# Kernel tuning notes

Hardware: AMD Instinct MI355X
Metric: run time of the kernel (lower is better)

Reference implementation:

```python
import jax, jax.numpy as jnp
import numpy as np

# Module constants (match init_kwargs / DCNv4 defaults)
N, C, H, W = 4, 256, 128, 128
G = 4                       # DCNv4 default group
KS = 3                      # kernel_size
K = KS * KS                 # 9 sampling points per group
Cg = C // G                 # channels per group
PAD_OFF = int(np.ceil(G * K * 3 / 8) * 8)  # 112, padded offset_mask dim
EPS = 1e-5                  # BatchNorm2d eps


def setup_inputs() -> dict:
    key = jax.random.key(0)
    ks = jax.random.split(key, 6)
    s = 0.05
    return {
        "x": jax.random.normal(ks[0], (N, C, H, W), jnp.float32),
        "conv_w": jax.random.normal(ks[1], (C, C, 1, 1), jnp.float32) * s,
        "bn1_gamma": jnp.ones((C,), jnp.float32),
        "bn1_beta": jnp.zeros((C,), jnp.float32),
        "bn1_mean": jnp.zeros((C,), jnp.float32),
        "bn1_var": jnp.ones((C,), jnp.float32),
        "value_w": jax.random.normal(ks[2], (C, C), jnp.float32) * s,
        "value_b": jnp.zeros((C,), jnp.float32),
        "offset_w": jax.random.normal(ks[3], (PAD_OFF, C), jnp.float32) * s,
        "offset_b": jnp.zeros((PAD_OFF,), jnp.float32),
        "out_w": jax.random.normal(ks[4], (C, C), jnp.float32) * s,
        "out_b": jnp.zeros((C,), jnp.float32),
        "bn2_gamma": jnp.ones((C,), jnp.float32),
        "bn2_beta": jnp.zeros((C,), jnp.float32),
        "bn2_mean": jnp.zeros((C,), jnp.float32),
        "bn2_var": jnp.ones((C,), jnp.float32),
    }


def _bilinear(v, lh, lw):
    """Bilinear sample v:(N,H,W,G,Cg) at float locs lh/lw:(N,H,W,G); zero outside."""
    n, h, w, g, c = v.shape
    h0 = jnp.floor(lh)
    w0 = jnp.floor(lw)
    dh = lh - h0
    dw = lw - w0
    h0i = h0.astype(jnp.int32)
    w0i = w0.astype(jnp.int32)
    vf = v.reshape(n, h * w, g, c)

    def gather(hh, ww):
        valid = (hh >= 0) & (hh < h) & (ww >= 0) & (ww < w)
        idx = jnp.clip(hh, 0, h - 1) * w + jnp.clip(ww, 0, w - 1)
        out = jnp.take_along_axis(vf, idx.reshape(n, h * w, g)[..., None], axis=1)
        return out.reshape(n, h, w, g, c) * valid[..., None].astype(v.dtype)

    w00 = (1 - dh) * (1 - dw)
    w01 = (1 - dh) * dw
    w10 = dh * (1 - dw)
    w11 = dh * dw
    return (gather(h0i, w0i) * w00[..., None]
            + gather(h0i, w0i + 1) * w01[..., None]
            + gather(h0i + 1, w0i) * w10[..., None]
            + gather(h0i + 1, w0i + 1) * w11[..., None])


def _bn(x_nchw, gamma, beta, mean, var):
    scale = (gamma / jnp.sqrt(var + EPS))[None, :, None, None]
    return x_nchw * scale + (beta - mean * gamma / jnp.sqrt(var + EPS))[None, :, None, None]


def reference(x, conv_w, bn1_gamma, bn1_beta, bn1_mean, bn1_var,
              value_w, value_b, offset_w, offset_b, out_w, out_b,
              bn2_gamma, bn2_beta, bn2_mean, bn2_var):
    n, _, h, w = x.shape
    # ---- Conv(c1,c2,k=1): 1x1 conv (no bias) + BN + SiLU ----
    y = jnp.einsum('nchw,oc->nohw', x, conv_w[:, :, 0, 0])
    y = jax.nn.silu(_bn(y, bn1_gamma, bn1_beta, bn1_mean, bn1_var))

    # ---- DCNv4 on (N, L, C) tokens ----
    t = y.transpose(0, 2, 3, 1)                      # (N,H,W,C)
    v = t @ value_w.T + value_b                      # value_proj
    om = t @ offset_w.T + offset_b                   # (N,H,W,112)
    om = om[..., : G * K * 3].reshape(n, h, w, G, K * 3)
    off = om[..., : 2 * K].reshape(n, h, w, G, K, 2) # (dx, dy) per point
    mask = om[..., 2 * K:]                           # (N,H,W,G,K), no softmax in v4
    v = v.reshape(n, h, w, G, Cg)

    hi = jnp.arange(h, dtype=jnp.float32)[None, :, None, None]
    wi = jnp.arange(w, dtype=jnp.float32)[None, None, :, None]
    out = jnp.zeros_like(v)
    for k in range(K):  # fixed small kernel loop (9 points)
        i, j = divmod(k, KS)
        lh = hi + (i - 1) + off[..., k, 1]           # stride=1, pad=1, dil=1
        lw = wi + (j - 1) + off[..., k, 0]           # offset_scale=1.0
        out = out + mask[..., k, None] * _bilinear(v, lh, lw)

    o = out.reshape(n, h, w, C) @ out_w.T + out_b    # output_proj
    o = o.transpose(0, 3, 1, 2)                      # back to NCHW

    # ---- final BN + SiLU ----
    return jax.nn.silu(_bn(o, bn2_gamma, bn2_beta, bn2_mean, bn2_var))
```

## Files before the change

### kernel.cpp

```cpp
#include <hip/hip_runtime.h>
#include <cstdint>

typedef unsigned short u16;
typedef unsigned int   u32;
typedef __attribute__((ext_vector_type(8))) __bf16 bf16x8;
typedef __attribute__((ext_vector_type(2))) float  f32x2;
typedef __attribute__((ext_vector_type(4))) float  f32x4;
typedef __attribute__((ext_vector_type(4))) u32    u32x4;

#define N_IMG 4
#define C_DIM 256
#define H_DIM 128
#define W_DIM 128
#define HW    (H_DIM * W_DIM)
#define M_TOT (N_IMG * HW)
#define CG    64
#define PADOFF 112
#define EPSV  1e-5f

__device__ __forceinline__ u16 f2b(float f) {
  u32 u = __float_as_uint(f);
  u += 0x7fffu + ((u >> 16) & 1u);
  return (u16)(u >> 16);
}

__device__ __forceinline__ void async_cp16(const void* g, void* l) {
  __builtin_amdgcn_global_load_lds(
      (const __attribute__((address_space(1))) void*)g,
      (__attribute__((address_space(3))) void*)l, 16, 0, 0);
}

__global__ __launch_bounds__(256) void cast_all(
    const float* __restrict__ a0, u16* __restrict__ o0,
    const float* __restrict__ a1, u16* __restrict__ o1,
    const float* __restrict__ a2, u16* __restrict__ o2,
    const float* __restrict__ a3, u16* __restrict__ o3) {
  int i = blockIdx.x * 256 + threadIdx.x;
  const float* in; u16* out; int base;
  if (i < 16384)      { in = a0; out = o0; base = 0; }
  else if (i < 32768) { in = a1; out = o1; base = 16384; }
  else if (i < 39936) { in = a2; out = o2; base = 32768; }
  else                { in = a3; out = o3; base = 39936; }
  int j = i - base;
  f32x4 v = reinterpret_cast<const f32x4*>(in)[j];
  u32 lo = (u32)f2b(v[0]) | ((u32)f2b(v[1]) << 16);
  u32 hi = (u32)f2b(v[2]) | ((u32)f2b(v[3]) << 16);
  reinterpret_cast<u32*>(out)[2 * j]     = lo;
  reinterpret_cast<u32*>(out)[2 * j + 1] = hi;
}

__global__ __launch_bounds__(256) void gemm_conv(
    const float* __restrict__ X, const u16* __restrict__ B,
    u16* __restrict__ Cb,
    const float* __restrict__ gamma, const float* __restrict__ beta,
    const float* __restrict__ mean, const float* __restrict__ var) {
  constexpr int BM = 128, BK = 32;
  __shared__ __align__(16) u16 As[BM * BK];
  __shared__ __align__(16) u16 Bs[BM * BK];
  const int tid  = threadIdx.x;
  const int lane = tid & 63;
  const int wave = tid >> 6;
  const int quad = lane >> 4;
  const int l16  = lane & 15;
  const int bm = blockIdx.x * BM;
  const int bn = blockIdx.y * BM;
  const int wm = (wave & 1) * 64;
  const int wn = (wave >> 1) * 64;
  const int img = bm >> 14;
  const int hw0 = bm & (HW - 1);
  const int p2  = (tid & 63) * 2;
  const int hh  = tid >> 6;
  const float* xb = X + (size_t)img * C_DIM * HW + hw0 + p2;

  f32x4 acc[4][4] = {};

  for (int ko = 0; ko < C_DIM; ko += BK) {
    float a0[8], a1[8];
#pragma unroll
    for (int j = 0; j < 8; ++j) {
      f32x2 fv = *reinterpret_cast<const f32x2*>(
          xb + (size_t)(ko + hh * 8 + j) * HW);
      a0[j] = fv.x; a1[j] = fv.y;
    }
    u32x4 w0, w1;
#pragma unroll
    for (int j = 0; j < 4; ++j) {
      w0[j] = (u32)f2b(a0[2 * j]) | ((u32)f2b(a0[2 * j + 1]) << 16);
      w1[j] = (u32)f2b(a1[2 * j]) | ((u32)f2b(a1[2 * j + 1]) << 16);
    }
    {
      u32x4* Ar = reinterpret_cast<u32x4*>(As);
      int sw = hh ^ ((p2 >> 1) & 3);
      Ar[p2 * 4 + sw]       = w0;
      Ar[(p2 + 1) * 4 + sw] = w1;
    }
#pragma unroll
    for (int it = 0; it < 2; ++it) {
      int chunk = it * 256 + tid;
      int r  = chunk >> 2;
      int kk = (chunk & 3) << 3;
      async_cp16(B + (size_t)(bn + r) * C_DIM + (ko + kk),
                 Bs + (size_t)(it * 256 + wave * 64) * 8);
    }
    __syncthreads();
    const bf16x8* Apf = reinterpret_cast<const bf16x8*>(As);
    const bf16x8* Bpf = reinterpret_cast<const bf16x8*>(Bs);
    bf16x8 af[4], bfr[4];
#pragma unroll
    for (int mi = 0; mi < 4; ++mi) {
      int r = wm + mi * 16 + l16;
      af[mi] = Apf[r * 4 + (quad ^ ((r >> 1) & 3))];
    }
#pragma unroll
    for (int ni = 0; ni < 4; ++ni)
      bfr[ni] = Bpf[(wn + ni * 16 + l16) * 4 + quad];
#pragma unroll
    for (int mi = 0; mi < 4; ++mi)
#pragma unroll
      for (int ni = 0; ni < 4; ++ni)
        acc[mi][ni] = __builtin_amdgcn_mfma_f32_16x16x32_bf16(
            af[mi], bfr[ni], acc[mi][ni], 0, 0, 0);
    __syncthreads();
  }

#pragma unroll
  for (int ni = 0; ni < 4; ++ni) {
    int n = bn + wn + ni * 16 + l16;
    float sc = gamma[n] * rsqrtf(var[n] + EPSV);
    float sh = beta[n] - mean[n] * sc;
#pragma unroll
    for (int mi = 0; mi < 4; ++mi) {
      int mrow = bm + wm + mi * 16 + quad * 4;
#pragma unroll
      for (int i = 0; i < 4; ++i) {
        float y = acc[mi][ni][i] * sc + sh;
        y = y / (1.f + __expf(-y));
        Cb[(size_t)(mrow + i) * C_DIM + n] = f2b(y);
      }
    }
  }
}

template <int MODE>
__global__ __launch_bounds__(256) void gemm_ep(
    const u16* __restrict__ A, const u16* __restrict__ B,
    u16* __restrict__ Cb, float* __restrict__ Cf, int K, int Nreal,
    const float* __restrict__ bias, const float* __restrict__ bias2,
    const float* __restrict__ gamma, const float* __restrict__ beta,
    const float* __restrict__ mean, const float* __restrict__ var) {
  constexpr int BM = 128, BK = 64;
  __shared__ __align__(16) u16 As[BM * BK];
  __shared__ __align__(16) u16 Bs[BM * BK];
  const int tid  = threadIdx.x;
  const int lane = tid & 63;
  const int wave = tid >> 6;
  const int quad = lane >> 4;
  const int l16  = lane & 15;
  const int bm = blockIdx.x * BM;
  const int bn = blockIdx.y * BM;
  const int wm = (wave & 1) * 64;
  const int wn = (wave >> 1) * 64;

  f32x4 acc[4][4] = {};

  for (int ko = 0; ko < K; ko += BK) {
#pragma unroll
    for (int it = 0; it < 4; ++it) {
      int chunk = it * 256 + tid;
      int r  = chunk >> 3;
      int j  = chunk & 7;
      int kk = (j ^ (r & 7)) << 3;
      const u16* ga = A + (size_t)(bm + r) * K + (ko + kk);
      int br = bn + r; if (br >= Nreal) br = Nreal - 1;
      const u16* gb = B + (size_t)br * K + (ko + kk);
      u16* la = As + (size_t)(it * 256 + wave * 64) * 8;
      u16* lb = Bs + (size_t)(it * 256 + wave * 64) * 8;
      async_cp16(ga, la);
      async_cp16(gb, lb);
    }
    __syncthreads();
    const bf16x8* Ap = reinterpret_cast<const bf16x8*>(As);
    const bf16x8* Bp = reinterpret_cast<const bf16x8*>(Bs);
#pragma unroll
    for (int ks = 0; ks < 2; ++ks) {
      bf16x8 af[4], bfr[4];
#pragma unroll
      for (int mi = 0; mi < 4; ++mi) {
        int row = wm + mi * 16 + l16;
        af[mi] = Ap[row * 8 + ((ks * 4 + quad) ^ (row & 7))];
      }
#pragma unroll
      for (int ni = 0; ni < 4; ++ni) {
        int row = wn + ni * 16 + l16;
        bfr[ni] = Bp[row * 8 + ((ks * 4 + quad) ^ (row & 7))];
      }
#pragma unroll
      for (int mi = 0; mi < 4; ++mi)
#pragma unroll
        for (int ni = 0; ni < 4; ++ni)
          acc[mi][ni] = __builtin_amdgcn_mfma_f32_16x16x32_bf16(
              af[mi], bfr[ni], acc[mi][ni], 0, 0, 0);
    }
    __syncthreads();
  }

#pragma unroll
  for (int ni = 0; ni < 4; ++ni) {
    int n = bn + wn + ni * 16 + l16;
    if constexpr (MODE == 3) {
      float sc = gamma[n] * rsqrtf(var[n] + EPSV);
      float sh = beta[n] - mean[n] * sc + bias[n] * sc;
#pragma unroll
      for (int mi = 0; mi < 4; ++mi) {
        int mrow = bm + wm + mi * 16 + quad * 4;
        int img = mrow >> 14;
        int hw  = mrow & (HW - 1);
        f32x4 y;
#pragma unroll
        for (int i = 0; i < 4; ++i) {
          float z = acc[mi][ni][i] * sc + sh;
          y[i] = z / (1.f + __expf(-z));
        }
        *reinterpret_cast<f32x4*>(
            Cf + (size_t)img * C_DIM * HW + (size_t)n * HW + hw) = y;
      }
    } else {
      if (bn < C_DIM) {
        float sh = bias[n];
#pragma unroll
        for (int mi = 0; mi < 4; ++mi) {
          int mrow = bm + wm + mi * 16 + quad * 4;
#pragma unroll
          for (int i = 0; i < 4; ++i)
            Cb[(size_t)(mrow + i) * C_DIM + n] = f2b(acc[mi][ni][i] + sh);
        }
      } else {
        int col = n - C_DIM;
        bool ok = col < PADOFF;
        float sh = ok ? bias2[col] : 0.f;
#pragma unroll
        for (int mi = 0; mi < 4; ++mi) {
          int mrow = bm + wm + mi * 16 + quad * 4;
#pragma unroll
          for (int i = 0; i < 4; ++i)
            if (ok) Cf[(size_t)(mrow + i) * PADOFF + col] = acc[mi][ni][i] + sh;
        }
      }
    }
  }
}

__global__ __launch_bounds__(256) void dcn_sample(
    const u16* __restrict__ v, const float* __restrict__ om,
    u16* __restrict__ outp) {
  __shared__ float sm[16 * PADOFF];
  const int tid = threadIdx.x;
  const int bid = blockIdx.x;
  const int cpx = gridDim.x >> 3;
  const int wg  = (bid & 7) * cpx + (bid >> 3);
  const int m0  = wg * 16;
  {
    const float* src = om + (size_t)m0 * PADOFF;
#pragma unroll
    for (int i = 0; i < 7; ++i) sm[tid + i * 256] = src[tid + i * 256];
  }
  __syncthreads();
  const int c4 = tid & 3;
  const int g  = (tid >> 2) & 3;
  const int pl = tid >> 4;
  const int m  = m0 + pl;
  const int n  = m >> 14;
  const int hw = m & (HW - 1);
  const int h = hw >> 7, w = hw & 127;
  const float* p = sm + pl * PADOFF + g * 27;
  const u16* vb = v + (size_t)n * HW * C_DIM + g * CG + c4 * 16;
  float acc[16] = {};
#pragma unroll
  for (int k = 0; k < 9; ++k) {
    const int di = k / 3 - 1, dj = k % 3 - 1;
    float ox = p[2 * k], oy = p[2 * k + 1], mk = p[18 + k];
    float lh = (float)(h + di) + oy;
    float lw = (float)(w + dj) + ox;
    float fh = floorf(lh), fw = floorf(lw);
    float dh = lh - fh, dw = lw - fw;
    int h0 = (int)fh, w0 = (int)fw;
    float wy0 = (1.f - dh) * mk, wy1 = dh * mk;
    float wx0 = 1.f - dw, wx1 = dw;
    bool okw0 = (u32)w0 < (u32)W_DIM;
    bool okw1 = (u32)(w0 + 1) < (u32)W_DIM;
    int w0c = min(max(w0, 0), W_DIM - 1);
    int w1c = min(max(w0 + 1, 0), W_DIM - 1);
#pragma unroll
    for (int cy = 0; cy < 2; ++cy) {
      int hh = h0 + cy;
      bool okh = (u32)hh < (u32)H_DIM;
      int hc = min(max(hh, 0), H_DIM - 1);
      const u16* rowp = vb + (size_t)(hc << 7) * C_DIM;
      const u16* qA = rowp + (size_t)w0c * C_DIM;
      const u16* qB = rowp + (size_t)w1c * C_DIM;
      u32x4 a0 = *reinterpret_cast<const u32x4*>(qA);
      u32x4 a1 = *reinterpret_cast<const u32x4*>(qA + 8);
      u32x4 b0 = *reinterpret_cast<const u32x4*>(qB);
      u32x4 b1 = *reinterpret_cast<const u32x4*>(qB + 8);
      float wyc = (cy == 0) ? wy0 : wy1;
      float wtA = (okh && okw0) ? wyc * wx0 : 0.f;
      float wtB = (okh && okw1) ? wyc * wx1 : 0.f;
      u32 wp;
      asm("v_cvt_pk_bf16_f32 %0, %1, %2" : "=v"(wp) : "v"(wtA), "v"(wtB));
#pragma unroll
      for (int j = 0; j < 4; ++j) {
        u32 lo0 = __builtin_amdgcn_perm(a0[j], b0[j], 0x01000504u);
        u32 hi0 = __builtin_amdgcn_perm(a0[j], b0[j], 0x03020706u);
        u32 lo1 = __builtin_amdgcn_perm(a1[j], b1[j], 0x01000504u);
        u32 hi1 = __builtin_amdgcn_perm(a1[j], b1[j], 0x03020706u);
        asm("v_dot2_f32_bf16 %0, %1, %2, %3"
            : "=v"(acc[2 * j]) : "v"(lo0), "v"(wp), "v"(acc[2 * j]));
        asm("v_dot2_f32_bf16 %0, %1, %2, %3"
            : "=v"(acc[2 * j + 1]) : "v"(hi0), "v"(wp), "v"(acc[2 * j + 1]));
        asm("v_dot2_f32_bf16 %0, %1, %2, %3"
            : "=v"(acc[8 + 2 * j]) : "v"(lo1), "v"(wp), "v"(acc[8 + 2 * j]));
        asm("v_dot2_f32_bf16 %0, %1, %2, %3"
            : "=v"(acc[8 + 2 * j + 1]) : "v"(hi1), "v"(wp), "v"(acc[8 + 2 * j + 1]));
      }
    }
  }
  u32x4 r0, r1;
#pragma unroll
  for (int j = 0; j < 4; ++j) {
    u32 pa, pb;
    asm("v_cvt_pk_bf16_f32 %0, %1, %2"
        : "=v"(pa) : "v"(acc[2 * j]), "v"(acc[2 * j + 1]));
    asm("v_cvt_pk_bf16_f32 %0, %1, %2"
        : "=v"(pb) : "v"(acc[8 + 2 * j]), "v"(acc[8 + 2 * j + 1]));
    r0[j] = pa; r1[j] = pb;
  }
  u16* o = outp + (size_t)m * C_DIM + g * CG + c4 * 16;
  *reinterpret_cast<u32x4*>(o)     = r0;
  *reinterpret_cast<u32x4*>(o + 8) = r1;
}

extern "C" void kernel_launch(void* const* d_in, const int* in_sizes, int n_in,
                              void* d_out, int out_size, void* d_ws, size_t ws_size,
                              hipStream_t stream) {
  const float* x        = (const float*)d_in[0];
  const float* conv_w   = (const float*)d_in[1];
  const float* bn1_g    = (const float*)d_in[2];
  const float* bn1_b    = (const float*)d_in[3];
  const float* bn1_m    = (const float*)d_in[4];
  const float* bn1_v    = (const float*)d_in[5];
  const float* value_w  = (const float*)d_in[6];
  const float* value_b  = (const float*)d_in[7];
  const float* offset_w = (const float*)d_in[8];
  const float* offset_b = (const float*)d_in[9];
  const float* out_w    = (const float*)d_in[10];
  const float* out_b    = (const float*)d_in[11];
  const float* bn2_g    = (const float*)d_in[12];
  const float* bn2_b    = (const float*)d_in[13];
  const float* bn2_m    = (const float*)d_in[14];
  const float* bn2_v    = (const float*)d_in[15];

  char* ws = (char*)d_ws;
  u16*   dcn  = (u16*)(ws);
  u16*   t    = (u16*)(ws + 33554432);
  u16*   vv   = (u16*)(ws + 67108864);
  float* om   = (float*)(ws + 100663296);
  u16*   wc   = (u16*)(ws + 130023424);
  u16*   wcat = (u16*)(ws + 130154496);
  u16*   wout = (u16*)(ws + 130342912);
  float* outp = (float*)d_out;

  cast_all<<<220, 256, 0, stream>>>(conv_w, wc, value_w, wcat,
                                    offset_w, wcat + 65536, out_w, wout);

  gemm_conv<<<dim3(M_TOT / 128, 2), 256, 0, stream>>>(
      x, wc, t, bn1_g, bn1_b, bn1_m, bn1_v);
  gemm_ep<1><<<dim3(M_TOT / 128, 3), 256, 0, stream>>>(
      t, wcat, vv, om, C_DIM, C_DIM + PADOFF,
      value_b, offset_b, nullptr, nullptr, nullptr, nullptr);
  dcn_sample<<<dim3(M_TOT / 16), 256, 0, stream>>>(vv, om, dcn);
  gemm_ep<3><<<dim3(M_TOT / 128, 2), 256, 0, stream>>>(
      dcn, wout, nullptr, outp, C_DIM, C_DIM,
      out_b, nullptr, bn2_g, bn2_b, bn2_m, bn2_v);
}
```

Before: 270.0 us.

## Fuse 1x1 conv GEMM with value/offset projection via LDS-resident tile

Merges the conv+BN+SiLU GEMM and the value/offset projection GEMM into one kernel. Each block computes a full 128x256 activation tile and keeps it in a 64KB LDS buffer, then runs the concatenated value/offset GEMM from LDS. This removes the global write and reread of the intermediate tensor and one launch. In exchange the input activations are no longer split across two blocks in N, so the grid shrinks from two or three blocks per row tile to one. The large LDS footprint also limits occupancy to roughly one or two blocks per CU.

New measurement: 254.9 us. 1.06x faster.

```diff
diff --git a/kernel.cpp b/kernel.cpp
--- a/kernel.cpp
+++ b/kernel.cpp
@@ -16,6 +16,7 @@
 #define M_TOT (N_IMG * HW)
 #define CG    64
 #define PADOFF 112
+#define NCAT  368
 #define EPSV  1e-5f
 
 __device__ __forceinline__ u16 f2b(float f) {
@@ -49,12 +50,15 @@
   reinterpret_cast<u32*>(out)[2 * j + 1] = hi;
 }
 
-__global__ __launch_bounds__(256) void gemm_conv(
-    const float* __restrict__ X, const u16* __restrict__ B,
-    u16* __restrict__ Cb,
+__global__ __launch_bounds__(256) void fused_proj(
+    const float* __restrict__ X, const u16* __restrict__ Bc,
+    const u16* __restrict__ Wcat,
+    u16* __restrict__ Vv, float* __restrict__ Om,
+    const float* __restrict__ vbias, const float* __restrict__ obias,
     const float* __restrict__ gamma, const float* __restrict__ beta,
     const float* __restrict__ mean, const float* __restrict__ var) {
   constexpr int BM = 128, BK = 32;
+  __shared__ __align__(16) u16 T[BM * C_DIM];
   __shared__ __align__(16) u16 As[BM * BK];
   __shared__ __align__(16) u16 Bs[BM * BK];
   const int tid  = threadIdx.x;
@@ -63,7 +67,6 @@
   const int quad = lane >> 4;
   const int l16  = lane & 15;
   const int bm = blockIdx.x * BM;
-  const int bn = blockIdx.y * BM;
   const int wm = (wave & 1) * 64;
   const int wn = (wave >> 1) * 64;
   const int img = bm >> 14;
@@ -72,80 +75,143 @@
   const int hh  = tid >> 6;
   const float* xb = X + (size_t)img * C_DIM * HW + hw0 + p2;
 
-  f32x4 acc[4][4] = {};
-
-  for (int ko = 0; ko < C_DIM; ko += BK) {
-    float a0[8], a1[8];
-#pragma unroll
-    for (int j = 0; j < 8; ++j) {
-      f32x2 fv = *reinterpret_cast<const f32x2*>(
-          xb + (size_t)(ko + hh * 8 + j) * HW);
-      a0[j] = fv.x; a1[j] = fv.y;
-    }
-    u32x4 w0, w1;
-#pragma unroll
-    for (int j = 0; j < 4; ++j) {
-      w0[j] = (u32)f2b(a0[2 * j]) | ((u32)f2b(a0[2 * j + 1]) << 16);
-      w1[j] = (u32)f2b(a1[2 * j]) | ((u32)f2b(a1[2 * j + 1]) << 16);
-    }
-    {
-      u32x4* Ar = reinterpret_cast<u32x4*>(As);
-      int sw = hh ^ ((p2 >> 1) & 3);
-      Ar[p2 * 4 + sw]       = w0;
-      Ar[(p2 + 1) * 4 + sw] = w1;
-    }
-#pragma unroll
-    for (int it = 0; it < 2; ++it) {
-      int chunk = it * 256 + tid;
-      int r  = chunk >> 2;
-      int kk = (chunk & 3) << 3;
-      async_cp16(B + (size_t)(bn + r) * C_DIM + (ko + kk),
-                 Bs + (size_t)(it * 256 + wave * 64) * 8);
-    }
-    __syncthreads();
-    const bf16x8* Apf = reinterpret_cast<const bf16x8*>(As);
-    const bf16x8* Bpf = reinterpret_cast<const bf16x8*>(Bs);
-    bf16x8 af[4], bfr[4];
-#pragma unroll
-    for (int mi = 0; mi < 4; ++mi) {
-      int r = wm + mi * 16 + l16;
-      af[mi] = Apf[r * 4 + (quad ^ ((r >> 1) & 3))];
-    }
-#pragma unroll
-    for (int ni = 0; ni < 4; ++ni)
-      bfr[ni] = Bpf[(wn + ni * 16 + l16) * 4 + quad];
-#pragma unroll
-    for (int mi = 0; mi < 4; ++mi)
+  for (int ny = 0; ny < 2; ++ny) {
+    const int bn = ny * 128;
+    f32x4 acc[4][4] = {};
+    for (int ko = 0; ko < C_DIM; ko += BK) {
+      float a0[8], a1[8];
+#pragma unroll
+      for (int j = 0; j < 8; ++j) {
+        f32x2 fv = *reinterpret_cast<const f32x2*>(
+            xb + (size_t)(ko + hh * 8 + j) * HW);
+        a0[j] = fv.x; a1[j] = fv.y;
+      }
+      u32x4 w0, w1;
+#pragma unroll
+      for (int j = 0; j < 4; ++j) {
+        w0[j] = (u32)f2b(a0[2 * j]) | ((u32)f2b(a0[2 * j + 1]) << 16);
+        w1[j] = (u32)f2b(a1[2 * j]) | ((u32)f2b(a1[2 * j + 1]) << 16);
+      }
+      {
+        u32x4* Ar = reinterpret_cast<u32x4*>(As);
+        int sw = hh ^ ((p2 >> 1) & 3);
+        Ar[p2 * 4 + sw]       = w0;
+        Ar[(p2 + 1) * 4 + sw] = w1;
+      }
+#pragma unroll
+      for (int it = 0; it < 2; ++it) {
+        int chunk = it * 256 + tid;
+        int r  = chunk >> 2;
+        int kk = (chunk & 3) << 3;
+        async_cp16(Bc + (size_t)(bn + r) * C_DIM + (ko + kk),
+                   Bs + (size_t)(it * 256 + wave * 64) * 8);
+      }
+      __syncthreads();
+      const bf16x8* Apf = reinterpret_cast<const bf16x8*>(As);
+      const bf16x8* Bpf = reinterpret_cast<const bf16x8*>(Bs);
+      bf16x8 af[4], bfr[4];
+#pragma unroll
+      for (int mi = 0; mi < 4; ++mi) {
+        int r = wm + mi * 16 + l16;
+        af[mi] = Apf[r * 4 + (quad ^ ((r >> 1) & 3))];
+      }
 #pragma unroll
       for (int ni = 0; ni < 4; ++ni)
-        acc[mi][ni] = __builtin_amdgcn_mfma_f32_16x16x32_bf16(
-            af[mi], bfr[ni], acc[mi][ni], 0, 0, 0);
-    __syncthreads();
-  }
-
-#pragma unroll
-  for (int ni = 0; ni < 4; ++ni) {
-    int n = bn + wn + ni * 16 + l16;
-    float sc = gamma[n] * rsqrtf(var[n] + EPSV);
-    float sh = beta[n] - mean[n] * sc;
-#pragma unroll
-    for (int mi = 0; mi < 4; ++mi) {
-      int mrow = bm + wm + mi * 16 + quad * 4;
-#pragma unroll
-      for (int i = 0; i < 4; ++i) {
-        float y = acc[mi][ni][i] * sc + sh;
-        y = y / (1.f + __expf(-y));
-        Cb[(size_t)(mrow + i) * C_DIM + n] = f2b(y);
-      }
-    }
-  }
-}
-
-template <int MODE>
-__global__ __launch_bounds__(256) void gemm_ep(
+        bfr[ni] = Bpf[(wn + ni * 16 + l16) * 4 + quad];
+#pragma unroll
+      for (int mi = 0; mi < 4; ++mi)
+#pragma unroll
+        for (int ni = 0; ni < 4; ++ni)
+          acc[mi][ni] = __builtin_amdgcn_mfma_f32_16x16x32_bf16(
+              af[mi], bfr[ni], acc[mi][ni], 0, 0, 0);
+      __syncthreads();
+    }
+#pragma unroll
+    for (int ni = 0; ni < 4; ++ni) {
+      int n = bn + wn + ni * 16 + l16;
+      float sc = gamma[n] * rsqrtf(var[n] + EPSV);
+      float sh = beta[n] - mean[n] * sc;
+#pragma unroll
+      for (int mi = 0; mi < 4; ++mi) {
+        int row = wm + mi * 16 + quad * 4;
+#pragma unroll
+        for (int i = 0; i < 4; ++i) {
+          float y = acc[mi][ni][i] * sc + sh;
+          y = y / (1.f + __expf(-y));
+          int rr = row + i;
+          T[rr * C_DIM + (((n >> 3) ^ (rr & 15)) << 3) + (n & 7)] = f2b(y);
+        }
+      }
+    }
+  }
+  __syncthreads();
+
+  for (int nc = 0; nc < 3; ++nc) {
+    const int n0 = nc * 128;
+    f32x4 acc[4][4] = {};
+    for (int ko = 0; ko < C_DIM; ko += BK) {
+#pragma unroll
+      for (int it = 0; it < 2; ++it) {
+        int chunk = it * 256 + tid;
+        int r  = chunk >> 2;
+        int kk = (chunk & 3) << 3;
+        int br = n0 + r; if (br >= NCAT) br = NCAT - 1;
+        async_cp16(Wcat + (size_t)br * C_DIM + (ko + kk),
+                   Bs + (size_t)(it * 256 + wave * 64) * 8);
+      }
+      __syncthreads();
+      const bf16x8* Bpf = reinterpret_cast<const bf16x8*>(Bs);
+      bf16x8 af[4], bfr[4];
+#pragma unroll
+      for (int mi = 0; mi < 4; ++mi) {
+        int row = wm + mi * 16 + l16;
+        int ch  = (ko >> 3) + quad;
+        af[mi] = *reinterpret_cast<const bf16x8*>(
+            &T[row * C_DIM + ((ch ^ (row & 15)) << 3)]);
+      }
+#pragma unroll
+      for (int ni = 0; ni < 4; ++ni)
+        bfr[ni] = Bpf[(wn + ni * 16 + l16) * 4 + quad];
+#pragma unroll
+      for (int mi = 0; mi < 4; ++mi)
+#pragma unroll
+        for (int ni = 0; ni < 4; ++ni)
+          acc[mi][ni] = __builtin_amdgcn_mfma_f32_16x16x32_bf16(
+              af[mi], bfr[ni], acc[mi][ni], 0, 0, 0);
+      __syncthreads();
+    }
+#pragma unroll
+    for (int ni = 0; ni < 4; ++ni) {
+      int n = n0 + wn + ni * 16 + l16;
+      if (n < C_DIM) {
+        float sh = vbias[n];
+#pragma unroll
+        for (int mi = 0; mi < 4; ++mi) {
+          int mrow = bm + wm + mi * 16 + quad * 4;
+#pragma unroll
+          for (int i = 0; i < 4; ++i)
+            Vv[(size_t)(mrow + i) * C_DIM + n] = f2b(acc[mi][ni][i] + sh);
+        }
+      } else {
+        int col = n - C_DIM;
+        bool ok = col < PADOFF;
+        float sh = ok ? obias[col] : 0.f;
+#pragma unroll
+        for (int mi = 0; mi < 4; ++mi) {
+          int mrow = bm + wm + mi * 16 + quad * 4;
+#pragma unroll
+          for (int i = 0; i < 4; ++i)
+            if (ok) Om[(size_t)(mrow + i) * PADOFF + col] = acc[mi][ni][i] + sh;
+        }
+      }
+    }
+  }
+}
+
+__global__ __launch_bounds__(256) void gemm_out(
     const u16* __restrict__ A, const u16* __restrict__ B,
-    u16* __restrict__ Cb, float* __restrict__ Cf, int K, int Nreal,
-    const float* __restrict__ bias, const float* __restrict__ bias2,
+    float* __restrict__ Cf,
+    const float* __restrict__ bias,
     const float* __restrict__ gamma, const float* __restrict__ beta,
     const float* __restrict__ mean, const float* __restrict__ var) {
   constexpr int BM = 128, BK = 64;
@@ -163,20 +229,17 @@
 
   f32x4 acc[4][4] = {};
 
-  for (int ko = 0; ko < K; ko += BK) {
+  for (int ko = 0; ko < C_DIM; ko += BK) {
 #pragma unroll
     for (int it = 0; it < 4; ++it) {
       int chunk = it * 256 + tid;
       int r  = chunk >> 3;
       int j  = chunk & 7;
       int kk = (j ^ (r & 7)) << 3;
-      const u16* ga = A + (size_t)(bm + r) * K + (ko + kk);
-      int br = bn + r; if (br >= Nreal) br = Nreal - 1;
-      const u16* gb = B + (size_t)br * K + (ko + kk);
-      u16* la = As + (size_t)(it * 256 + wave * 64) * 8;
-      u16* lb = Bs + (size_t)(it * 256 + wave * 64) * 8;
-      async_cp16(ga, la);
-      async_cp16(gb, lb);
+      async_cp16(A + (size_t)(bm + r) * C_DIM + (ko + kk),
+                 As + (size_t)(it * 256 + wave * 64) * 8);
+      async_cp16(B + (size_t)(bn + r) * C_DIM + (ko + kk),
+                 Bs + (size_t)(it * 256 + wave * 64) * 8);
     }
     __syncthreads();
     const bf16x8* Ap = reinterpret_cast<const bf16x8*>(As);
@@ -207,45 +270,21 @@
 #pragma unroll
   for (int ni = 0; ni < 4; ++ni) {
     int n = bn + wn + ni * 16 + l16;
-    if constexpr (MODE == 3) {
-      float sc = gamma[n] * rsqrtf(var[n] + EPSV);
-      float sh = beta[n] - mean[n] * sc + bias[n] * sc;
-#pragma unroll
-      for (int mi = 0; mi < 4; ++mi) {
-        int mrow = bm + wm + mi * 16 + quad * 4;
-        int img = mrow >> 14;
-        int hw  = mrow & (HW - 1);
-        f32x4 y;
-#pragma unroll
-        for (int i = 0; i < 4; ++i) {
-          float z = acc[mi][ni][i] * sc + sh;
-          y[i] = z / (1.f + __expf(-z));
-        }
-        *reinterpret_cast<f32x4*>(
-            Cf + (size_t)img * C_DIM * HW + (size_t)n * HW + hw) = y;
-      }
-    } else {
-      if (bn < C_DIM) {
-        float sh = bias[n];
-#pragma unroll
-        for (int mi = 0; mi < 4; ++mi) {
-          int mrow = bm + wm + mi * 16 + quad * 4;
-#pragma unroll
-          for (int i = 0; i < 4; ++i)
-            Cb[(size_t)(mrow + i) * C_DIM + n] = f2b(acc[mi][ni][i] + sh);
-        }
-      } else {
-        int col = n - C_DIM;
-        bool ok = col < PADOFF;
-        float sh = ok ? bias2[col] : 0.f;
-#pragma unroll
-        for (int mi = 0; mi < 4; ++mi) {
-          int mrow = bm + wm + mi * 16 + quad * 4;
-#pragma unroll
-          for (int i = 0; i < 4; ++i)
-            if (ok) Cf[(size_t)(mrow + i) * PADOFF + col] = acc[mi][ni][i] + sh;
-        }
-      }
+    float sc = gamma[n] * rsqrtf(var[n] + EPSV);
+    float sh = beta[n] - mean[n] * sc + bias[n] * sc;
+#pragma unroll
+    for (int mi = 0; mi < 4; ++mi) {
+      int mrow = bm + wm + mi * 16 + quad * 4;
+      int img = mrow >> 14;
+      int hw  = mrow & (HW - 1);
+      f32x4 y;
+#pragma unroll
+      for (int i = 0; i < 4; ++i) {
+        float z = acc[mi][ni][i] * sc + sh;
+        y[i] = z / (1.f + __expf(-z));
+      }
+      *reinterpret_cast<f32x4*>(
+          Cf + (size_t)img * C_DIM * HW + (size_t)n * HW + hw) = y;
     }
   }
 }
@@ -360,25 +399,21 @@
   const float* bn2_v    = (const float*)d_in[15];
 
   char* ws = (char*)d_ws;
-  u16*   dcn  = (u16*)(ws);
-  u16*   t    = (u16*)(ws + 33554432);
-  u16*   vv   = (u16*)(ws + 67108864);
-  float* om   = (float*)(ws + 100663296);
-  u16*   wc   = (u16*)(ws + 130023424);
-  u16*   wcat = (u16*)(ws + 130154496);
-  u16*   wout = (u16*)(ws + 130342912);
+  u16*   vv   = (u16*)(ws);
+  float* om   = (float*)(ws + 33554432);
+  u16*   dcn  = (u16*)(ws + 67108864);
+  u16*   wc   = (u16*)(ws + 100663296);
+  u16*   wcat = (u16*)(ws + 100794368);
+  u16*   wout = (u16*)(ws + 100982784);
   float* outp = (float*)d_out;
 
   cast_all<<<220, 256, 0, stream>>>(conv_w, wc, value_w, wcat,
                                     offset_w, wcat + 65536, out_w, wout);
 
-  gemm_conv<<<dim3(M_TOT / 128, 2), 256, 0, stream>>>(
-      x, wc, t, bn1_g, bn1_b, bn1_m, bn1_v);
-  gemm_ep<1><<<dim3(M_TOT / 128, 3), 256, 0, stream>>>(
-      t, wcat, vv, om, C_DIM, C_DIM + PADOFF,
-      value_b, offset_b, nullptr, nullptr, nullptr, nullptr);
+  fused_proj<<<dim3(M_TOT / 128), 256, 0, stream>>>(
+      x, wc, wcat, vv, om, value_b, offset_b,
+      bn1_g, bn1_b, bn1_m, bn1_v);
   dcn_sample<<<dim3(M_TOT / 16), 256, 0, stream>>>(vv, om, dcn);
-  gemm_ep<3><<<dim3(M_TOT / 128, 2), 256, 0, stream>>>(
-      dcn, wout, nullptr, outp, C_DIM, C_DIM,
-      out_b, nullptr, bn2_g, bn2_b, bn2_m, bn2_v);
-}
+  gemm_out<<<dim3(M_TOT / 128, 2), 256, 0, stream>>>(
+      dcn, wout, outp, out_b, bn2_g, bn2_b, bn2_m, bn2_v);
+}
```
